# Performance work log

Hardware: AMD Instinct MI355X
Metric: run time of the kernel (lower is better)

Reference implementation:

```python
import jax, jax.numpy as jnp
import numpy as np

NUM_BINS = 8
TAIL = 3.0
MBW = 0.001  # min_bin_width
MBH = 0.001  # min_bin_height
MD = 0.001   # min_derivative


def _conv(x, w, b):
    y = jax.lax.conv_general_dilated(x, w, (1, 1), 'SAME',
                                     dimension_numbers=('NCHW', 'OIHW', 'NCHW'))
    return y + b[None, :, None, None]


def _convnet(x, w1, b1, w2, b2, w3, b3):
    h = jax.nn.relu(_conv(x, w1, b1))
    h = jax.nn.relu(_conv(h, w2, b2))
    return _conv(h, w3, b3)


def _rqs_forward(x, uw, uh, ud):
    # x: (N,), uw/uh: (N, num_bins), ud: (N, num_bins-1)
    nb = uw.shape[-1]
    inside = (x >= -TAIL) & (x <= TAIL)
    xin = jnp.clip(x, -TAIL, TAIL)
    # linear tails: pad derivatives so boundary slope == 1
    const = float(np.log(np.exp(1.0 - MD) - 1.0))
    ud = jnp.pad(ud, ((0, 0), (1, 1)), constant_values=const)

    widths = jax.nn.softmax(uw, axis=-1)
    widths = MBW + (1.0 - MBW * nb) * widths
    cumw = jnp.pad(jnp.cumsum(widths, axis=-1), ((0, 0), (1, 0)))
    cumw = 2.0 * TAIL * cumw - TAIL
    cumw = cumw.at[:, 0].set(-TAIL).at[:, -1].set(TAIL)
    widths = cumw[:, 1:] - cumw[:, :-1]

    heights = jax.nn.softmax(uh, axis=-1)
    heights = MBH + (1.0 - MBH * nb) * heights
    cumh = jnp.pad(jnp.cumsum(heights, axis=-1), ((0, 0), (1, 0)))
    cumh = 2.0 * TAIL * cumh - TAIL
    cumh = cumh.at[:, 0].set(-TAIL).at[:, -1].set(TAIL)
    heights = cumh[:, 1:] - cumh[:, :-1]

    deriv = MD + jax.nn.softplus(ud)  # (N, nb+1)

    # searchsorted: locate bin of each element
    idx = jnp.clip(jnp.sum((xin[:, None] >= cumw).astype(jnp.int32), axis=-1) - 1, 0, nb - 1)
    gather = lambda t: jnp.take_along_axis(t, idx[:, None], axis=-1)[:, 0]

    in_cw = gather(cumw)
    in_w = gather(widths)
    in_ch = gather(cumh)
    in_h = gather(heights)
    in_delta = gather(heights / widths)
    d0 = gather(deriv)
    d1 = gather(deriv[:, 1:])

    theta = (xin - in_cw) / in_w
    tom = theta * (1.0 - theta)
    numer = in_h * (in_delta * theta ** 2 + d0 * tom)
    denom = in_delta + (d0 + d1 - 2.0 * in_delta) * tom
    y = in_ch + numer / denom
    dnum = in_delta ** 2 * (d1 * theta ** 2 + 2.0 * in_delta * tom + d0 * (1.0 - theta) ** 2)
    lad = jnp.log(dnum) - 2.0 * jnp.log(denom)

    y = jnp.where(inside, y, x)
    lad = jnp.where(inside, lad, 0.0)
    return y, lad


def setup_inputs() -> dict:
    key = jax.random.key(0)
    ks = jax.random.split(key, 9)
    B, C, H, W = 32, 12, 64, 64
    hidden = 128
    cond_c = C // 3
    out_spline = C * (3 * NUM_BINS - 1)
    x = jax.random.normal(ks[0], (B, C, H, W), dtype=jnp.float32)
    logdet = jnp.zeros((B,), dtype=jnp.float32)
    conditioning = jax.random.normal(ks[1], (B, cond_c, H, W), dtype=jnp.float32)
    w1 = jax.random.normal(ks[2], (hidden, C + cond_c, 3, 3), dtype=jnp.float32) * 0.05
    b1 = jnp.zeros((hidden,), dtype=jnp.float32)
    w2 = jax.random.normal(ks[3], (hidden, hidden, 1, 1), dtype=jnp.float32) * 0.05
    b2 = jnp.zeros((hidden,), dtype=jnp.float32)
    w3 = jax.random.normal(ks[4], (out_spline, hidden, 3, 3), dtype=jnp.float32) * 0.01
    b3 = jnp.zeros((out_spline,), dtype=jnp.float32)
    return {"x": x, "logdet": logdet, "conditioning": conditioning,
            "w1": w1, "b1": b1, "w2": w2, "b2": b2, "w3": w3, "b3": b3}


def reference(x, logdet, conditioning, w1, b1, w2, b2, w3, b3):
    B, C, H, W = x.shape
    net_in = jnp.concatenate([x, conditioning], axis=1)
    params = _convnet(net_in, w1, b1, w2, b2, w3, b3)  # (B, C*(3nb-1), H, W)
    params = params.reshape(B, C, 3 * NUM_BINS - 1, H, W)
    params = params.transpose(0, 1, 3, 4, 2).reshape(B * C * H * W, 3 * NUM_BINS - 1)
    uw = params[:, :NUM_BINS]
    uh = params[:, NUM_BINS:2 * NUM_BINS]
    ud = params[:, 2 * NUM_BINS:]
    y_flat, lad_flat = _rqs_forward(x.reshape(-1), uw, uh, ud)
    y = y_flat.reshape(B, C, H, W)
    logdet_out = logdet + lad_flat.reshape(B, -1).sum(axis=1)
    return y, logdet_out
```

## Files before the change

kernel.cpp:

```cpp
#include <hip/hip_runtime.h>
#include <math.h>


#define NPIX 4096
#define NY   1572864

typedef _Float16 half8 __attribute__((ext_vector_type(8)));
typedef _Float16 half4 __attribute__((ext_vector_type(4)));
typedef float f32x4 __attribute__((ext_vector_type(4)));

#define ASYNC16(gsrc, ldst) \
  __builtin_amdgcn_global_load_lds((const __attribute__((address_space(1))) unsigned int*)(gsrc), \
                                   (__attribute__((address_space(3))) unsigned int*)(ldst), 16, 0, 0)

#define H2P_PLANE 4356
#define H2P_IDX(b, cc, pp) ((((size_t)(b) * 4 + (cc)) * H2P_PLANE + (pp)) << 5)
#define XH_IDX(b, pp) (((size_t)(b) * H2P_PLANE + (pp)) << 5)

__global__ __launch_bounds__(256) void prep_k(
    const float* __restrict__ w1, const float* __restrict__ w2,
    const float* __restrict__ w3, _Float16* __restrict__ w1h,
    _Float16* __restrict__ w2h, _Float16* __restrict__ w3h,
    const float* __restrict__ logdet, float* __restrict__ ld_out)
{
    const int i = blockIdx.x * 256 + threadIdx.x;
    if (i < 36864) {
        int k = i & 31, oc = (i >> 5) & 127, t = i >> 12;
        w1h[i] = (_Float16)((k < 16) ? w1[(oc * 16 + k) * 9 + t] : 0.f);
    }
    if (i < 16384) {
        int km = i & 31, oc = (i >> 5) & 127, ks = i >> 12;
        w2h[i] = (_Float16)w2[oc * 128 + ks * 32 + km];
    }
    {
        int cim = i & 31;
        int oc = (i >> 5) % 288;
        int tc = i / (288 * 32);
        int t = tc >> 2, cc = tc & 3;
        int c = oc / 24, j = oc % 24;
        int ci = cc * 32 + cim;
        float v = (j < 23) ? w3[((c * 23 + j) * 128 + ci) * 9 + t] : 0.f;
        w3h[i] = (_Float16)v;
    }
    if (i < 32) ld_out[i] = logdet[i];
}

__global__ __launch_bounds__(256) void xh_k(
    const float* __restrict__ x, const float* __restrict__ cond,
    _Float16* __restrict__ xh)
{
    const int i = blockIdx.x * 256 + threadIdx.x;
    if (i >= 139392) return;
    const int b = i / H2P_PLANE, pp = i % H2P_PLANE;
    const int pr = pp / 66, pc = pp % 66;
    const bool interior = (pr >= 1) && (pr <= 64) && (pc >= 1) && (pc <= 64);
    _Float16 v[32];
#pragma unroll
    for (int ci = 0; ci < 32; ++ci) v[ci] = (_Float16)0.f;
    if (interior) {
        const int p = (pr - 1) * 64 + (pc - 1);
#pragma unroll
        for (int ci = 0; ci < 12; ++ci)
            v[ci] = (_Float16)x[((size_t)(b * 12 + ci) << 12) + p];
#pragma unroll
        for (int ci = 0; ci < 4; ++ci)
            v[12 + ci] = (_Float16)cond[((size_t)(b * 4 + ci) << 12) + p];
    }
    _Float16* dst = xh + ((size_t)i << 5);
#pragma unroll
    for (int q = 0; q < 4; ++q) *(f32x4*)(dst + q * 8) = *(f32x4*)(v + q * 8);
}

__global__ __launch_bounds__(256) void zring_k(_Float16* __restrict__ h2p)
{
    const int i = blockIdx.x * 256 + threadIdx.x;
    if (i >= 133120) return;
    const int q = i & 3;
    const int rest = i >> 2;
    const int r = rest % 260;
    const int cc = (rest / 260) & 3;
    const int b = rest / 1040;
    int pp;
    if (r < 66)       pp = r;
    else if (r < 132) pp = 65 * 66 + (r - 66);
    else if (r < 196) pp = (r - 131) * 66;
    else              pp = (r - 195) * 66 + 65;
    f32x4 z = {0.f, 0.f, 0.f, 0.f};
    *(f32x4*)(h2p + H2P_IDX(b, cc, pp) + q * 8) = z;
}

__global__ __launch_bounds__(256, 2) void conv1_k(
    const _Float16* __restrict__ xh, const _Float16* __restrict__ w1h,
    const float* __restrict__ b1, _Float16* __restrict__ h1p)
{
    __shared__ __align__(16) char smem[73728];
    const int tid = threadIdx.x;
    const int wv = tid >> 6, lane = tid & 63;
    const int row16 = lane & 15, quad = lane >> 4;
    const int ptile = blockIdx.x;
    const int b = ptile >> 4;
    const int pim0 = (ptile & 15) << 8;
    const int h0 = pim0 >> 6;

#pragma unroll
    for (int k = 0; k < 18; ++k)
        ASYNC16(w1h + (size_t)(k * 256 + tid) * 8, smem + (k * 256 + wv * 64) * 16);

    f32x4 acc[4][8];
#pragma unroll
    for (int pt = 0; pt < 4; ++pt)
#pragma unroll
        for (int ot = 0; ot < 8; ++ot) acc[pt][ot] = (f32x4){0.f, 0.f, 0.f, 0.f};

    __syncthreads();
    const _Float16* wl = (const _Float16*)smem;

    for (int t = 0; t < 9; ++t) {
        const int dy = t / 3, dx = t % 3;
        const int pbase = (h0 + wv + dy) * 66 + dx + row16;
        half8 bf[4], af[8];
#pragma unroll
        for (int pt = 0; pt < 4; ++pt)
            bf[pt] = *(const half8*)(xh + XH_IDX(b, pbase + pt * 16) + quad * 8);
#pragma unroll
        for (int ot = 0; ot < 8; ++ot)
            af[ot] = *(const half8*)(wl + ((t * 128 + ot * 16 + row16) << 5) + quad * 8);
#pragma unroll
        for (int ot = 0; ot < 8; ++ot)
#pragma unroll
            for (int pt = 0; pt < 4; ++pt)
                acc[pt][ot] = __builtin_amdgcn_mfma_f32_16x16x32_f16(af[ot], bf[pt], acc[pt][ot], 0, 0, 0);
    }

    f32x4 bias[8];
#pragma unroll
    for (int ot = 0; ot < 8; ++ot) bias[ot] = *(const f32x4*)(b1 + ot * 16 + quad * 4);
#pragma unroll
    for (int pt = 0; pt < 4; ++pt) {
        const size_t pbase = ((size_t)((b << 12) + pim0 + wv * 64 + pt * 16 + row16)) << 7;
#pragma unroll
        for (int ot = 0; ot < 8; ++ot) {
            half4 v;
#pragma unroll
            for (int r = 0; r < 4; ++r)
                v[r] = (_Float16)fmaxf(acc[pt][ot][r] + bias[ot][r], 0.f);
            *(half4*)(h1p + pbase + ot * 16 + quad * 4) = v;
        }
    }
}

__global__ __launch_bounds__(256, 2) void conv2_k(
    const _Float16* __restrict__ h1p, const _Float16* __restrict__ w2h,
    const float* __restrict__ b2, _Float16* __restrict__ h2p)
{
    __shared__ __align__(16) char smem[33280];
    float* b2l = (float*)(smem + 32768);
    const int tid = threadIdx.x;
    const int wv = tid >> 6, lane = tid & 63;
    const int row16 = lane & 15, quad = lane >> 4;
    const int ptile = blockIdx.x;
    const int b = ptile >> 4;
    const int pim0 = (ptile & 15) << 8;

    if (tid < 128) b2l[tid] = b2[tid];
#pragma unroll
    for (int k = 0; k < 8; ++k) {
        const int c0 = k * 256 + wv * 64;
        ASYNC16(w2h + (size_t)(c0 + lane) * 8, smem + c0 * 16);
    }

    f32x4 acc[4][8];
#pragma unroll
    for (int pt = 0; pt < 4; ++pt)
#pragma unroll
        for (int ot = 0; ot < 8; ++ot) acc[pt][ot] = (f32x4){0.f, 0.f, 0.f, 0.f};

    const int pixbase = (b << 12) + pim0 + wv * 64;
    __syncthreads();

#pragma unroll
    for (int ks = 0; ks < 4; ++ks) {
        half8 bf[4], af[8];
#pragma unroll
        for (int pt = 0; pt < 4; ++pt)
            bf[pt] = *(const half8*)(h1p + ((size_t)(pixbase + pt * 16 + row16) << 7) + ks * 32 + quad * 8);
        const _Float16* wl = (const _Float16*)smem;
#pragma unroll
        for (int ot = 0; ot < 8; ++ot)
            af[ot] = *(const half8*)(wl + ((ks * 128 + ot * 16 + row16) << 5) + quad * 8);
#pragma unroll
        for (int ot = 0; ot < 8; ++ot)
#pragma unroll
            for (int pt = 0; pt < 4; ++pt)
                acc[pt][ot] = __builtin_amdgcn_mfma_f32_16x16x32_f16(af[ot], bf[pt], acc[pt][ot], 0, 0, 0);
    }

#pragma unroll
    for (int pt = 0; pt < 4; ++pt) {
        const int p = pim0 + wv * 64 + pt * 16 + row16;
        const int pp = ((p >> 6) + 1) * 66 + (p & 63) + 1;
#pragma unroll
        for (int ot = 0; ot < 8; ++ot) {
            const int oc0 = ot * 16 + quad * 4;
            half4 v;
#pragma unroll
            for (int r = 0; r < 4; ++r)
                v[r] = (_Float16)fmaxf(acc[pt][ot][r] + b2l[oc0 + r], 0.f);
            *(half4*)(h2p + H2P_IDX(b, oc0 >> 5, pp) + (oc0 & 31)) = v;
        }
    }
}

__device__ __forceinline__ void rqs_eval(const float* prm, float xv,
                                         float& yv_out, float& lad_out)
{
    const float xin = fminf(fmaxf(xv, -3.f), 3.f);

    float mw = prm[0], mh = prm[8];
#pragma unroll
    for (int j = 1; j < 8; ++j) { mw = fmaxf(mw, prm[j]); mh = fmaxf(mh, prm[8 + j]); }
    float ew[8], eh[8];
    float sw = 0.f, sh = 0.f;
#pragma unroll
    for (int j = 0; j < 8; ++j) {
        ew[j] = expf(prm[j] - mw);      sw += ew[j];
        eh[j] = expf(prm[8 + j] - mh);  sh += eh[j];
    }
    const float rw = 1.f / sw, rh = 1.f / sh;

    const float CONST_D = logf(expf(0.999f) - 1.f);

    float cumw = 0.f, cumh = 0.f;
    float cw_lo = -3.f, ch_lo = -3.f;
    float in_cw = 0.f, in_w = 1.f, in_ch = 0.f, in_h = 1.f, sd0 = 0.f, sd1 = 0.f;
#pragma unroll
    for (int i = 0; i < 8; ++i) {
        cumw += fmaf(0.992f, ew[i] * rw, 0.001f);
        cumh += fmaf(0.992f, eh[i] * rh, 0.001f);
        const float cw_hi = (i == 7) ? 3.f : fmaf(6.f, cumw, -3.f);
        const float ch_hi = (i == 7) ? 3.f : fmaf(6.f, cumh, -3.f);
        const bool sel = (xin >= cw_lo) && ((i == 7) || (xin < cw_hi));
        in_cw = sel ? cw_lo : in_cw;
        in_w  = sel ? (cw_hi - cw_lo) : in_w;
        in_ch = sel ? ch_lo : in_ch;
        in_h  = sel ? (ch_hi - ch_lo) : in_h;
        sd0   = sel ? ((i == 0) ? CONST_D : prm[16 + i - 1]) : sd0;
        sd1   = sel ? ((i == 7) ? CONST_D : prm[16 + i]) : sd1;
        cw_lo = cw_hi; ch_lo = ch_hi;
    }

    const float d0 = 0.001f + ((sd0 > 20.f) ? sd0 : log1pf(expf(sd0)));
    const float d1 = 0.001f + ((sd1 > 20.f) ? sd1 : log1pf(expf(sd1)));

    const float delta = in_h / in_w;
    const float theta = (xin - in_cw) / in_w;
    const float omt = 1.f - theta;
    const float tom = theta * omt;
    const float th2 = theta * theta;
    const float numer = in_h * (delta * th2 + d0 * tom);
    const float denom = delta + (d0 + d1 - 2.f * delta) * tom;
    float yv = in_ch + numer / denom;
    const float dnum = delta * delta * (d1 * th2 + 2.f * delta * tom + d0 * omt * omt);
    float lad = logf(dnum) - 2.f * logf(denom);

    const bool inside = (xv >= -3.f) && (xv <= 3.f);
    yv_out = inside ? yv : xv;
    lad_out = inside ? lad : 0.f;
}

__global__ __launch_bounds__(256, 2) void conv3_rqs_k(
    const _Float16* __restrict__ h2p, const _Float16* __restrict__ w3h,
    const float* __restrict__ b3, const float* __restrict__ x,
    float* __restrict__ y, float* __restrict__ ld_out)
{
    __shared__ __align__(16) char smem[44352];
    float* b3l = (float*)(smem + 43776);

    const int tid = threadIdx.x;
    const int wv = tid >> 6, lane = tid & 63;
    const int row16 = lane & 15, quad = lane >> 4;
    const int col = blockIdx.x;
    const int ptile = blockIdx.y;
    const int b = ptile >> 4;
    const int pim0 = (ptile & 15) << 8;
    const int h0 = pim0 >> 6;

    if (tid < 144) {
        const int c = tid / 24, j = tid % 24;
        b3l[tid] = (j < 23) ? b3[(col * 6 + c) * 23 + j] : 0.f;
    }

    f32x4 acc[4][9];
#pragma unroll
    for (int pt = 0; pt < 4; ++pt)
#pragma unroll
        for (int ot = 0; ot < 9; ++ot) acc[pt][ot] = (f32x4){0.f, 0.f, 0.f, 0.f};

    auto stage_wt = [&](int t, int cc, int buf) {
        const _Float16* g = w3h + ((size_t)((t * 4 + cc) * 288 + col * 144) << 5);
        char* wb = smem + 25344 + buf * 9216;
        ASYNC16(g + (size_t)tid * 8, wb + wv * 64 * 16);
        ASYNC16(g + (size_t)(256 + tid) * 8, wb + (256 + wv * 64) * 16);
        if (wv == 0) ASYNC16(g + (size_t)(512 + lane) * 8, wb + 512 * 16);
    };
    auto stage_act = [&](int cc) {
        const _Float16* ga = h2p + H2P_IDX(b, cc, h0 * 66);
#pragma unroll
        for (int k = 0; k < 6; ++k)
            ASYNC16(ga + (size_t)(k * 256 + tid) * 8, smem + (k * 256 + wv * 64) * 16);
        if (wv == 0 && lane < 48)
            ASYNC16(ga + (size_t)(1536 + lane) * 8, smem + 1536 * 16);
    };

    stage_act(0);
    stage_wt(0, 0, 0);

    for (int cc = 0; cc < 4; ++cc) {
        for (int t = 0; t < 9; ++t) {
            const int step = cc * 9 + t;
            __syncthreads();
            if (step + 1 < 36)
                stage_wt((t == 8) ? 0 : t + 1, (t == 8) ? cc + 1 : cc, (step + 1) & 1);
            const _Float16* act = (const _Float16*)smem;
            const _Float16* wt = (const _Float16*)(smem + 25344 + (step & 1) * 9216);
            const int dy = t / 3, dx = t % 3;
            const int lpp = (wv + dy) * 66 + dx + row16;
            half8 bf[4], af[9];
#pragma unroll
            for (int pt = 0; pt < 4; ++pt)
                bf[pt] = *(const half8*)(act + ((lpp + pt * 16) << 5) + quad * 8);
#pragma unroll
            for (int ot = 0; ot < 9; ++ot)
                af[ot] = *(const half8*)(wt + ((ot * 16 + row16) << 5) + quad * 8);
#pragma unroll
            for (int ot = 0; ot < 9; ++ot)
#pragma unroll
                for (int pt = 0; pt < 4; ++pt)
                    acc[pt][ot] = __builtin_amdgcn_mfma_f32_16x16x32_f16(af[ot], bf[pt], acc[pt][ot], 0, 0, 0);
            if (t == 8 && cc < 3) {
                __syncthreads();
                stage_act(cc + 1);
            }
        }
    }
    __syncthreads();

    float* epi = (float*)smem + wv * 2368;
    float lad_acc = 0.f;
#pragma unroll
    for (int pt = 0; pt < 4; ++pt) {
#pragma unroll
        for (int ot = 0; ot < 9; ++ot)
            *(f32x4*)(epi + row16 * 148 + ot * 16 + quad * 4) = acc[pt][ot];
        __syncthreads();
#pragma unroll 1
        for (int pass = 0; pass < 2; ++pass) {
            const int idx = pass * 64 + lane;
            if (idx < 96) {
                const int p16 = idx & 15, c = idx >> 4;
                float prm[23];
#pragma unroll
                for (int j = 0; j < 23; ++j)
                    prm[j] = epi[p16 * 148 + c * 24 + j] + b3l[c * 24 + j];
                const int tpix = wv * 64 + pt * 16 + p16;
                const size_t xi = (((size_t)(b * 12 + col * 6 + c)) << 12) + (pim0 + tpix);
                const float xv = x[xi];
                float yv, lad;
                rqs_eval(prm, xv, yv, lad);
                y[xi] = yv;
                lad_acc += lad;
            }
        }
        __syncthreads();
    }

#pragma unroll
    for (int off = 32; off > 0; off >>= 1) lad_acc += __shfl_down(lad_acc, off);
    if (lane == 0) atomicAdd(&ld_out[b], lad_acc);
}

extern "C" void kernel_launch(void* const* d_in, const int* in_sizes, int n_in,
                              void* d_out, int out_size, void* d_ws, size_t ws_size,
                              hipStream_t stream)
{
    const float* x      = (const float*)d_in[0];
    const float* logdet = (const float*)d_in[1];
    const float* cond   = (const float*)d_in[2];
    const float* w1     = (const float*)d_in[3];
    const float* b1     = (const float*)d_in[4];
    const float* w2     = (const float*)d_in[5];
    const float* b2     = (const float*)d_in[6];
    const float* w3     = (const float*)d_in[7];
    const float* b3     = (const float*)d_in[8];

    char* ws = (char*)d_ws;
    _Float16* h1p = (_Float16*)ws;
    _Float16* h2p = (_Float16*)(ws + 33554432);
    _Float16* xh  = (_Float16*)(ws + 33554432);
    _Float16* w1h = (_Float16*)(ws + 69238784);
    _Float16* w2h = (_Float16*)(ws + 69312512);
    _Float16* w3h = (_Float16*)(ws + 69345280);

    float* y      = (float*)d_out;
    float* ld_out = y + NY;

    prep_k<<<1296, 256, 0, stream>>>(w1, w2, w3, w1h, w2h, w3h, logdet, ld_out);
    xh_k<<<545, 256, 0, stream>>>(x, cond, xh);
    conv1_k<<<512, 256, 0, stream>>>(xh, w1h, b1, h1p);
    zring_k<<<520, 256, 0, stream>>>(h2p);
    conv2_k<<<512, 256, 0, stream>>>(h1p, w2h, b2, h2p);
    conv3_rqs_k<<<dim3(2, 512), 256, 0, stream>>>(h2p, w3h, b3, x, y, ld_out);
}
```

Before: 240.0 us.

## Swizzle LDS tile layouts for conflict-free MFMA reads and fold small kernels

Weight and activation tiles are now staged into LDS in a permuted order (gswt/gsa), so each lane's half8 fragment read lands in a contiguous, bank-friendly address instead of a 64-byte-strided one. This targets LDS bank conflicts in the MFMA inner loops of all three convolutions. Separately, the xh packing kernel is merged into the weight prep kernel and the h2p halo zeroing is moved into the tail of conv2, removing two kernel launches. The swizzle adds per-load index arithmetic on the async copies and makes correctness depend on matching read offsets.

```diff
diff --git a/kernel.cpp b/kernel.cpp
--- a/kernel.cpp
+++ b/kernel.cpp
@@ -13,15 +13,25 @@
   __builtin_amdgcn_global_load_lds((const __attribute__((address_space(1))) unsigned int*)(gsrc), \
                                    (__attribute__((address_space(3))) unsigned int*)(ldst), 16, 0, 0)
 
+__device__ __forceinline__ int gswt(int s) {
+    return (s & ~63) | ((s & 15) << 2) | ((s >> 4) & 3);
+}
+__device__ __forceinline__ int gsa(int s) {
+    int q = s / 396, p = s - q * 396;
+    return p * 4 + q;
+}
+
 #define H2P_PLANE 4356
 #define H2P_IDX(b, cc, pp) ((((size_t)(b) * 4 + (cc)) * H2P_PLANE + (pp)) << 5)
 #define XH_IDX(b, pp) (((size_t)(b) * H2P_PLANE + (pp)) << 5)
 
-__global__ __launch_bounds__(256) void prep_k(
+__global__ __launch_bounds__(256) void setup_k(
     const float* __restrict__ w1, const float* __restrict__ w2,
     const float* __restrict__ w3, _Float16* __restrict__ w1h,
     _Float16* __restrict__ w2h, _Float16* __restrict__ w3h,
-    const float* __restrict__ logdet, float* __restrict__ ld_out)
+    const float* __restrict__ logdet, float* __restrict__ ld_out,
+    const float* __restrict__ x, const float* __restrict__ cond,
+    _Float16* __restrict__ xh)
 {
     const int i = blockIdx.x * 256 + threadIdx.x;
     if (i < 36864) {
@@ -43,50 +53,26 @@
         w3h[i] = (_Float16)v;
     }
     if (i < 32) ld_out[i] = logdet[i];
-}
-
-__global__ __launch_bounds__(256) void xh_k(
-    const float* __restrict__ x, const float* __restrict__ cond,
-    _Float16* __restrict__ xh)
-{
-    const int i = blockIdx.x * 256 + threadIdx.x;
-    if (i >= 139392) return;
-    const int b = i / H2P_PLANE, pp = i % H2P_PLANE;
-    const int pr = pp / 66, pc = pp % 66;
-    const bool interior = (pr >= 1) && (pr <= 64) && (pc >= 1) && (pc <= 64);
-    _Float16 v[32];
-#pragma unroll
-    for (int ci = 0; ci < 32; ++ci) v[ci] = (_Float16)0.f;
-    if (interior) {
-        const int p = (pr - 1) * 64 + (pc - 1);
-#pragma unroll
-        for (int ci = 0; ci < 12; ++ci)
-            v[ci] = (_Float16)x[((size_t)(b * 12 + ci) << 12) + p];
-#pragma unroll
-        for (int ci = 0; ci < 4; ++ci)
-            v[12 + ci] = (_Float16)cond[((size_t)(b * 4 + ci) << 12) + p];
-    }
-    _Float16* dst = xh + ((size_t)i << 5);
-#pragma unroll
-    for (int q = 0; q < 4; ++q) *(f32x4*)(dst + q * 8) = *(f32x4*)(v + q * 8);
-}
-
-__global__ __launch_bounds__(256) void zring_k(_Float16* __restrict__ h2p)
-{
-    const int i = blockIdx.x * 256 + threadIdx.x;
-    if (i >= 133120) return;
-    const int q = i & 3;
-    const int rest = i >> 2;
-    const int r = rest % 260;
-    const int cc = (rest / 260) & 3;
-    const int b = rest / 1040;
-    int pp;
-    if (r < 66)       pp = r;
-    else if (r < 132) pp = 65 * 66 + (r - 66);
-    else if (r < 196) pp = (r - 131) * 66;
-    else              pp = (r - 195) * 66 + 65;
-    f32x4 z = {0.f, 0.f, 0.f, 0.f};
-    *(f32x4*)(h2p + H2P_IDX(b, cc, pp) + q * 8) = z;
+    if (i < 139392) {
+        const int b = i / H2P_PLANE, pp = i % H2P_PLANE;
+        const int pr = pp / 66, pc = pp % 66;
+        const bool interior = (pr >= 1) && (pr <= 64) && (pc >= 1) && (pc <= 64);
+        _Float16 v[32];
+#pragma unroll
+        for (int ci = 0; ci < 32; ++ci) v[ci] = (_Float16)0.f;
+        if (interior) {
+            const int p = (pr - 1) * 64 + (pc - 1);
+#pragma unroll
+            for (int ci = 0; ci < 12; ++ci)
+                v[ci] = (_Float16)x[((size_t)(b * 12 + ci) << 12) + p];
+#pragma unroll
+            for (int ci = 0; ci < 4; ++ci)
+                v[12 + ci] = (_Float16)cond[((size_t)(b * 4 + ci) << 12) + p];
+        }
+        _Float16* dst = xh + ((size_t)i << 5);
+#pragma unroll
+        for (int q = 0; q < 4; ++q) *(f32x4*)(dst + q * 8) = *(f32x4*)(v + q * 8);
+    }
 }
 
 __global__ __launch_bounds__(256, 2) void conv1_k(
@@ -104,7 +90,7 @@
 
 #pragma unroll
     for (int k = 0; k < 18; ++k)
-        ASYNC16(w1h + (size_t)(k * 256 + tid) * 8, smem + (k * 256 + wv * 64) * 16);
+        ASYNC16(w1h + (size_t)gswt(k * 256 + tid) * 8, smem + (k * 256 + wv * 64) * 16);
 
     f32x4 acc[4][8];
 #pragma unroll
@@ -114,6 +100,7 @@
 
     __syncthreads();
     const _Float16* wl = (const _Float16*)smem;
+    const int fro = ((quad << 4) | row16) * 8;
 
     for (int t = 0; t < 9; ++t) {
         const int dy = t / 3, dx = t % 3;
@@ -124,7 +111,7 @@
             bf[pt] = *(const half8*)(xh + XH_IDX(b, pbase + pt * 16) + quad * 8);
 #pragma unroll
         for (int ot = 0; ot < 8; ++ot)
-            af[ot] = *(const half8*)(wl + ((t * 128 + ot * 16 + row16) << 5) + quad * 8);
+            af[ot] = *(const half8*)(wl + ((t * 8 + ot) << 9) + fro);
 #pragma unroll
         for (int ot = 0; ot < 8; ++ot)
 #pragma unroll
@@ -164,10 +151,8 @@
 
     if (tid < 128) b2l[tid] = b2[tid];
 #pragma unroll
-    for (int k = 0; k < 8; ++k) {
-        const int c0 = k * 256 + wv * 64;
-        ASYNC16(w2h + (size_t)(c0 + lane) * 8, smem + c0 * 16);
-    }
+    for (int k = 0; k < 8; ++k)
+        ASYNC16(w2h + (size_t)gswt(k * 256 + tid) * 8, smem + (k * 256 + wv * 64) * 16);
 
     f32x4 acc[4][8];
 #pragma unroll
@@ -176,6 +161,7 @@
         for (int ot = 0; ot < 8; ++ot) acc[pt][ot] = (f32x4){0.f, 0.f, 0.f, 0.f};
 
     const int pixbase = (b << 12) + pim0 + wv * 64;
+    const int fro = ((quad << 4) | row16) * 8;
     __syncthreads();
 
 #pragma unroll
@@ -187,7 +173,7 @@
         const _Float16* wl = (const _Float16*)smem;
 #pragma unroll
         for (int ot = 0; ot < 8; ++ot)
-            af[ot] = *(const half8*)(wl + ((ks * 128 + ot * 16 + row16) << 5) + quad * 8);
+            af[ot] = *(const half8*)(wl + ((ks * 8 + ot) << 9) + fro);
 #pragma unroll
         for (int ot = 0; ot < 8; ++ot)
 #pragma unroll
@@ -208,6 +194,20 @@
                 v[r] = (_Float16)fmaxf(acc[pt][ot][r] + b2l[oc0 + r], 0.f);
             *(half4*)(h2p + H2P_IDX(b, oc0 >> 5, pp) + (oc0 & 31)) = v;
         }
+    }
+
+    const int gidx = (ptile & 15) * 256 + tid;
+    const f32x4 z = {0.f, 0.f, 0.f, 0.f};
+#pragma unroll 1
+    for (int u = gidx; u < 4160; u += 4096) {
+        const int cc = u / 1040, r4 = u - cc * 1040;
+        const int r = r4 >> 2, q = r4 & 3;
+        int pp;
+        if (r < 66)       pp = r;
+        else if (r < 132) pp = 65 * 66 + (r - 66);
+        else if (r < 196) pp = (r - 131) * 66;
+        else              pp = (r - 195) * 66 + 65;
+        *(f32x4*)(h2p + H2P_IDX(b, cc, pp) + q * 8) = z;
     }
 }
 
@@ -299,21 +299,23 @@
     auto stage_wt = [&](int t, int cc, int buf) {
         const _Float16* g = w3h + ((size_t)((t * 4 + cc) * 288 + col * 144) << 5);
         char* wb = smem + 25344 + buf * 9216;
-        ASYNC16(g + (size_t)tid * 8, wb + wv * 64 * 16);
-        ASYNC16(g + (size_t)(256 + tid) * 8, wb + (256 + wv * 64) * 16);
-        if (wv == 0) ASYNC16(g + (size_t)(512 + lane) * 8, wb + 512 * 16);
+        ASYNC16(g + (size_t)gswt(tid) * 8, wb + wv * 64 * 16);
+        ASYNC16(g + (size_t)gswt(256 + tid) * 8, wb + (256 + wv * 64) * 16);
+        if (wv == 0) ASYNC16(g + (size_t)gswt(512 + lane) * 8, wb + 512 * 16);
     };
     auto stage_act = [&](int cc) {
         const _Float16* ga = h2p + H2P_IDX(b, cc, h0 * 66);
 #pragma unroll
         for (int k = 0; k < 6; ++k)
-            ASYNC16(ga + (size_t)(k * 256 + tid) * 8, smem + (k * 256 + wv * 64) * 16);
+            ASYNC16(ga + (size_t)gsa(k * 256 + tid) * 8, smem + (k * 256 + wv * 64) * 16);
         if (wv == 0 && lane < 48)
-            ASYNC16(ga + (size_t)(1536 + lane) * 8, smem + 1536 * 16);
+            ASYNC16(ga + (size_t)gsa(1536 + lane) * 8, smem + 1536 * 16);
     };
 
     stage_act(0);
     stage_wt(0, 0, 0);
+
+    const int fro = ((quad << 4) | row16) * 8;
 
     for (int cc = 0; cc < 4; ++cc) {
         for (int t = 0; t < 9; ++t) {
@@ -324,14 +326,14 @@
             const _Float16* act = (const _Float16*)smem;
             const _Float16* wt = (const _Float16*)(smem + 25344 + (step & 1) * 9216);
             const int dy = t / 3, dx = t % 3;
-            const int lpp = (wv + dy) * 66 + dx + row16;
+            const int lpp = quad * 396 + (wv + dy) * 66 + dx + row16;
             half8 bf[4], af[9];
 #pragma unroll
             for (int pt = 0; pt < 4; ++pt)
-                bf[pt] = *(const half8*)(act + ((lpp + pt * 16) << 5) + quad * 8);
+                bf[pt] = *(const half8*)(act + (lpp + pt * 16) * 8);
 #pragma unroll
             for (int ot = 0; ot < 9; ++ot)
-                af[ot] = *(const half8*)(wt + ((ot * 16 + row16) << 5) + quad * 8);
+                af[ot] = *(const half8*)(wt + (ot << 9) + fro);
 #pragma unroll
             for (int ot = 0; ot < 9; ++ot)
 #pragma unroll
@@ -404,10 +406,9 @@
     float* y      = (float*)d_out;
     float* ld_out = y + NY;
 
-    prep_k<<<1296, 256, 0, stream>>>(w1, w2, w3, w1h, w2h, w3h, logdet, ld_out);
-    xh_k<<<545, 256, 0, stream>>>(x, cond, xh);
+    setup_k<<<1296, 256, 0, stream>>>(w1, w2, w3, w1h, w2h, w3h, logdet, ld_out,
+                                      x, cond, xh);
     conv1_k<<<512, 256, 0, stream>>>(xh, w1h, b1, h1p);
-    zring_k<<<520, 256, 0, stream>>>(h2p);
     conv2_k<<<512, 256, 0, stream>>>(h1p, w2h, b2, h2p);
     conv3_rqs_k<<<dim3(2, 512), 256, 0, stream>>>(h2p, w3h, b3, x, y, ld_out);
 }
```

Result: no change. 241.2 us (+0.5%).
